# Optimization experiments

Measured on AMD Instinct MI355X. Metric: run time of the kernel, lower is better.

## Reference

```python
import jax, jax.numpy as jnp
import numpy as np

N_HEAD, D_MODEL, D_K, D_V = 8, 128, 16, 16
EPS = 1e-5


def entmax15(x):
    # 1.5-entmax along last axis (Peters & Martins 2019, exact sort-based algo)
    x = x * 0.5
    x = x - jnp.max(x, axis=-1, keepdims=True)
    xs = jnp.flip(jnp.sort(x, axis=-1), axis=-1)  # descending
    K = x.shape[-1]
    rho = jnp.arange(1, K + 1, dtype=x.dtype)
    mean = jnp.cumsum(xs, axis=-1) / rho
    mean_sq = jnp.cumsum(xs * xs, axis=-1) / rho
    delta = (1.0 - rho * (mean_sq - mean * mean)) / rho
    tau = mean - jnp.sqrt(jnp.clip(delta, 0.0))
    support = jnp.sum(tau <= xs, axis=-1, keepdims=True)  # support size k*
    tau_star = jnp.take_along_axis(tau, support - 1, axis=-1)
    p = jnp.clip(x - tau_star, 0.0)
    return p * p


def layer_norm(x, gamma, beta):
    mu = jnp.mean(x, axis=-1, keepdims=True)
    var = jnp.mean((x - mu) ** 2, axis=-1, keepdims=True)
    return gamma * (x - mu) * jax.lax.rsqrt(var + EPS) + beta


def setup_inputs() -> dict:
    key = jax.random.key(0)
    ks = jax.random.split(key, 24)
    B, Lq, Lk, D = 4, 1024, 2048, D_MODEL
    s = 0.05
    f = jax.random.normal
    return {
        "q": f(ks[0], (B, Lq, D), jnp.float32),
        "k": f(ks[1], (B, Lk, D), jnp.float32),
        "v": f(ks[2], (B, Lk, D), jnp.float32),
        "v_2": f(ks[3], (B, Lq, D), jnp.float32),
        "W_Q": f(ks[4], (D, N_HEAD * D_K)) * s, "b_Q": f(ks[5], (N_HEAD * D_K,)) * s,
        "W_K": f(ks[6], (D, N_HEAD * D_K)) * s, "b_K": f(ks[7], (N_HEAD * D_K,)) * s,
        "W_V": f(ks[8], (D, N_HEAD * D_V)) * s, "b_V": f(ks[9], (N_HEAD * D_V,)) * s,
        "W_V2": f(ks[10], (D, N_HEAD * D_V)) * s, "b_V2": f(ks[11], (N_HEAD * D_V,)) * s,
        "W_O": f(ks[12], (N_HEAD * D_V, D)) * s, "b_O": f(ks[13], (D,)) * s,
        "W_O2": f(ks[14], (N_HEAD * D_V, D)) * s, "b_O2": f(ks[15], (D,)) * s,
        "W_R": f(ks[16], (D, D)) * s,
        "W_R2": f(ks[17], (D, D)) * s,
        "gamma": jnp.ones((D,), jnp.float32),
        "beta": jnp.zeros((D,), jnp.float32),
    }


def reference(q, k, v, v_2, W_Q, b_Q, W_K, b_K, W_V, b_V, W_V2, b_V2,
              W_O, b_O, W_O2, b_O2, W_R, W_R2, gamma, beta):
    B, Lq, _ = q.shape
    Lk = k.shape[1]
    Q = (q @ W_Q + b_Q).reshape(B, Lq, N_HEAD, D_K)
    Kh = (k @ W_K + b_K).reshape(B, Lk, N_HEAD, D_K)
    V = (v @ W_V + b_V).reshape(B, Lk, N_HEAD, D_V)
    V2 = (v_2 @ W_V2 + b_V2).reshape(B, Lq, N_HEAD, D_V)
    # scores: [B, H, Lq, Lk]
    scores = jnp.einsum('bqhd,bkhd->bhqk', Q, Kh) / np.float32(np.sqrt(D_K))
    A = entmax15(scores)                              # normalize over Lk
    A2 = entmax15(jnp.swapaxes(scores, -2, -1))       # normalize over Lq
    out = jnp.einsum('bhqk,bkhd->bqhd', A, V).reshape(B, Lq, N_HEAD * D_V)
    out2 = jnp.einsum('bhkq,bqhd->bkhd', A2, V2).reshape(B, Lk, N_HEAD * D_V)
    # dropout is identity in eval mode; both branches use the SAME layer_norm params (as in source)
    out = jax.nn.relu(layer_norm(out @ W_O + b_O + q @ W_R, gamma, beta))
    out2 = jax.nn.relu(layer_norm(out2 @ W_O2 + b_O2 + k @ W_R2, gamma, beta))
    return (out, out2, A, A2)
```

## Files before the change

### kernel.cpp

```cpp
#include <hip/hip_runtime.h>

__global__ __launch_bounds__(128) void proj_all_kernel(
    const float* __restrict__ q, const float* __restrict__ k,
    const float* __restrict__ v, const float* __restrict__ v2,
    const float* __restrict__ W_Q, const float* __restrict__ b_Q,
    const float* __restrict__ W_K, const float* __restrict__ b_K,
    const float* __restrict__ W_V, const float* __restrict__ b_V,
    const float* __restrict__ W_V2, const float* __restrict__ b_V2,
    float* __restrict__ Qp, float* __restrict__ Kp,
    float* __restrict__ Vp, float* __restrict__ V2p)
{
  __shared__ float xs[4][128];
  int blk = blockIdx.x;
  const float *X, *W, *B; float* Y; int L, chunked, rb;
  if (blk < 1024)      { X = q;  W = W_Q;  B = b_Q;  Y = Qp;  L = 1024; chunked = 1; rb = blk; }
  else if (blk < 3072) { X = k;  W = W_K;  B = b_K;  Y = Kp;  L = 2048; chunked = 1; rb = blk - 1024; }
  else if (blk < 5120) { X = v;  W = W_V;  B = b_V;  Y = Vp;  L = 2048; chunked = 0; rb = blk - 3072; }
  else                 { X = v2; W = W_V2; B = b_V2; Y = V2p; L = 1024; chunked = 0; rb = blk - 5120; }
  rb *= 4;
  int c = threadIdx.x;
#pragma unroll
  for (int i = 0; i < 4; ++i)
    xs[i][c] = X[(size_t)(rb + i) * 128 + c];
  __syncthreads();
  float b = B[c];
  float a0 = b, a1 = b, a2 = b, a3 = b;
#pragma unroll 8
  for (int d = 0; d < 128; ++d) {
    float w = W[d * 128 + c];
    a0 = fmaf(xs[0][d], w, a0);
    a1 = fmaf(xs[1][d], w, a1);
    a2 = fmaf(xs[2][d], w, a2);
    a3 = fmaf(xs[3][d], w, a3);
  }
  int h = c >> 4, dd = c & 15;
  float av[4] = { a0, a1, a2, a3 };
#pragma unroll
  for (int i = 0; i < 4; ++i) {
    int row = rb + i;
    int bb = row / L;
    int l  = row - bb * L;
    if (chunked)
      Y[(((size_t)(bb * 8 + h) * 4 + (dd >> 2)) * L + l) * 4 + (dd & 3)] = av[i];
    else
      Y[((size_t)(bb * 8 + h) * L + l) * 16 + dd] = av[i];
  }
}

static __device__ __forceinline__ float hstep(float f, float s1, float cnt)
{
  float arg = fmaf(-cnt, f, s1 * s1);
  return (arg > 0.f) ? f / (s1 + sqrtf(arg)) : f / (2.f * s1);
}

template<int LROW, int LCOL>
__global__ __launch_bounds__(256) void attn_kernel(
    const float* __restrict__ RowM, const float* __restrict__ ColM,
    const float* __restrict__ ValM, float* __restrict__ Aout,
    float* __restrict__ OutWs)
{
  constexpr int J   = LCOL / 64;
  constexpr int CAP = 512;
  constexpr float Z = 1.0f;
  __shared__ float          sval[4][CAP];
  __shared__ unsigned short sidx[4][CAP];

  int ws   = threadIdx.x >> 6;
  int wid  = blockIdx.x * 4 + ws;
  int lane = threadIdx.x & 63;
  int bh   = wid / LROW;
  int r    = wid - bh * LROW;
  int bb   = bh >> 3, h = bh & 7;

  float qf[16];
  { const float* qb = RowM + (size_t)bh * LROW * 16;
#pragma unroll
    for (int d = 0; d < 16; ++d)
      qf[d] = qb[((size_t)(d >> 2) * LROW + r) * 4 + (d & 3)] * 0.125f;
  }

  float x[J];
  const float4* Cb = (const float4*)(ColM + (size_t)bh * LCOL * 16);
#pragma unroll
  for (int j = 0; j < J; ++j) {
    int kk = lane + 64 * j;
    float4 k0 = Cb[0 * LCOL + kk];
    float  s  = qf[0] * k0.x;
    s = fmaf(qf[1], k0.y, s); s = fmaf(qf[2], k0.z, s); s = fmaf(qf[3], k0.w, s);
    float4 k1 = Cb[1 * LCOL + kk];
    s = fmaf(qf[4], k1.x, s); s = fmaf(qf[5], k1.y, s);
    s = fmaf(qf[6], k1.z, s); s = fmaf(qf[7], k1.w, s);
    float4 k2 = Cb[2 * LCOL + kk];
    s = fmaf(qf[8], k2.x, s); s = fmaf(qf[9], k2.y, s);
    s = fmaf(qf[10], k2.z, s); s = fmaf(qf[11], k2.w, s);
    float4 k3 = Cb[3 * LCOL + kk];
    s = fmaf(qf[12], k3.x, s); s = fmaf(qf[13], k3.y, s);
    s = fmaf(qf[14], k3.z, s); s = fmaf(qf[15], k3.w, s);
    x[j] = s;
  }

  float m = -1e30f, sr = 0.f, qr = 0.f;
#pragma unroll
  for (int j = 0; j < J; ++j) {
    m = fmaxf(m, x[j]);
    sr += x[j];
    qr = fmaf(x[j], x[j], qr);
  }
#pragma unroll
  for (int off = 32; off >= 1; off >>= 1) {
    m  = fmaxf(m, __shfl_xor(m, off));
    sr += __shfl_xor(sr, off);
    qr += __shfl_xor(qr, off);
  }
  float mu  = sr * (1.f / (float)LCOL);
  float sig = sqrtf(fmaxf(qr * (1.f / (float)LCOL) - mu * mu, 0.f));
  float theta = fmaxf(fmaf(Z, sig, mu), m - 1.0f);

  float* arow = Aout + ((size_t)bh * LROW + r) * LCOL;
  const float* Vb = ValM + (size_t)bh * LCOL * 16;
  float* op = OutWs + ((size_t)bb * LROW + r) * 128 + h * 16;

  int c = 0;
#pragma unroll
  for (int j = 0; j < J; ++j) c += (x[j] > theta) ? 1 : 0;
  int i = c;
#pragma unroll
  for (int off = 1; off <= 32; off <<= 1) {
    int t = __shfl_up(i, off);
    if (lane >= off) i += t;
  }
  int base = i - c;
  int tot  = __shfl(i, 63);

  if (tot >= 1 && tot <= CAP) {
    int w = 0;
#pragma unroll
    for (int j = 0; j < J; ++j) {
      if (x[j] > theta) {
        sval[ws][base + w] = x[j];
        sidx[ws][base + w] = (unsigned short)(lane + 64 * j);
        ++w;
      }
    }
    __threadfence_block();

    float tau = theta;
    bool valid = true;
    for (int it = 0; it < 24; ++it) {
      float s1 = 0.f, s2 = 0.f;
      int cnt = 0;
      for (int i2 = lane; i2 < tot; i2 += 64) {
        float t = sval[ws][i2] - tau, r0 = fmaxf(t, 0.f);
        s1 += r0; s2 = fmaf(r0, r0, s2);
        cnt += __popcll(__ballot(t > 0.f));
      }
#pragma unroll
      for (int off = 32; off >= 1; off >>= 1) {
        s1 += __shfl_xor(s1, off);
        s2 += __shfl_xor(s2, off);
      }
      float f = s2 - 1.0f;
      if (it == 0 && f < -1e-6f) { valid = false; break; }
      if (f > 1e-6f && s1 > 1e-12f) tau += hstep(f, s1, (float)cnt);
      else break;
    }

    if (valid) {
#pragma unroll
      for (int j = 0; j < J; ++j) {
        int kk = lane + 64 * j;
        float t = fmaxf(x[j] - tau, 0.f);
        arow[kk] = t * t;
      }

      float acc[16];
#pragma unroll
      for (int d = 0; d < 16; ++d) acc[d] = 0.f;
      for (int i2 = lane; i2 < tot; i2 += 64) {
        float t = sval[ws][i2] - tau;
        if (t > 0.f) {
          float p = t * t;
          int kk = sidx[ws][i2];
          const float4* vp = (const float4*)(Vb + (size_t)kk * 16);
          float4 v0 = vp[0], v1 = vp[1], v2 = vp[2], v3 = vp[3];
          acc[0]  = fmaf(p, v0.x, acc[0]);  acc[1]  = fmaf(p, v0.y, acc[1]);
          acc[2]  = fmaf(p, v0.z, acc[2]);  acc[3]  = fmaf(p, v0.w, acc[3]);
          acc[4]  = fmaf(p, v1.x, acc[4]);  acc[5]  = fmaf(p, v1.y, acc[5]);
          acc[6]  = fmaf(p, v1.z, acc[6]);  acc[7]  = fmaf(p, v1.w, acc[7]);
          acc[8]  = fmaf(p, v2.x, acc[8]);  acc[9]  = fmaf(p, v2.y, acc[9]);
          acc[10] = fmaf(p, v2.z, acc[10]); acc[11] = fmaf(p, v2.w, acc[11]);
          acc[12] = fmaf(p, v3.x, acc[12]); acc[13] = fmaf(p, v3.y, acc[13]);
          acc[14] = fmaf(p, v3.z, acc[14]); acc[15] = fmaf(p, v3.w, acc[15]);
        }
      }
#pragma unroll
      for (int off = 32; off >= 1; off >>= 1)
#pragma unroll
        for (int d = 0; d < 16; ++d) acc[d] += __shfl_xor(acc[d], off);
      float vv = acc[0];
#pragma unroll
      for (int d = 1; d < 16; ++d)
        vv = (lane == d) ? acc[d] : vv;
      if (lane < 16) op[lane] = vv;
      return;
    }
  }

  float tau = m - 1.0f;
  bool done = false;
  for (int it = 0; it < 24; ++it) {
    float a1 = 0.f, a2 = 0.f;
    int ac = 0;
#pragma unroll
    for (int j = 0; j < J; ++j) {
      float t = x[j] - tau, r0 = fmaxf(t, 0.f);
      a1 += r0; a2 = fmaf(r0, r0, a2);
      ac += __popcll(__ballot(t > 0.f));
    }
#pragma unroll
    for (int off = 32; off >= 1; off >>= 1) {
      a1 += __shfl_xor(a1, off);
      a2 += __shfl_xor(a2, off);
    }
    float f = a2 - 1.0f;
    bool g = !done && (f > 1e-6f) && (a1 > 1e-12f);
    if (g) tau += hstep(f, a1, (float)ac); else done = true;
    if (done) break;
  }

  float acc[16];
#pragma unroll
  for (int d = 0; d < 16; ++d) acc[d] = 0.f;
#pragma unroll
  for (int j = 0; j < J; ++j) {
    int kk = lane + 64 * j;
    float t = fmaxf(x[j] - tau, 0.f), p = t * t;
    arow[kk] = p;
    const float4* vp = (const float4*)(Vb + (size_t)kk * 16);
    float4 v0 = vp[0], v1 = vp[1], v2 = vp[2], v3 = vp[3];
    acc[0]  = fmaf(p, v0.x, acc[0]);  acc[1]  = fmaf(p, v0.y, acc[1]);
    acc[2]  = fmaf(p, v0.z, acc[2]);  acc[3]  = fmaf(p, v0.w, acc[3]);
    acc[4]  = fmaf(p, v1.x, acc[4]);  acc[5]  = fmaf(p, v1.y, acc[5]);
    acc[6]  = fmaf(p, v1.z, acc[6]);  acc[7]  = fmaf(p, v1.w, acc[7]);
    acc[8]  = fmaf(p, v2.x, acc[8]);  acc[9]  = fmaf(p, v2.y, acc[9]);
    acc[10] = fmaf(p, v2.z, acc[10]); acc[11] = fmaf(p, v2.w, acc[11]);
    acc[12] = fmaf(p, v3.x, acc[12]); acc[13] = fmaf(p, v3.y, acc[13]);
    acc[14] = fmaf(p, v3.z, acc[14]); acc[15] = fmaf(p, v3.w, acc[15]);
  }
#pragma unroll
  for (int off = 32; off >= 1; off >>= 1)
#pragma unroll
    for (int d = 0; d < 16; ++d) acc[d] += __shfl_xor(acc[d], off);
  float vv = acc[0];
#pragma unroll
  for (int d = 1; d < 16; ++d)
    vv = (lane == d) ? acc[d] : vv;
  if (lane < 16) op[lane] = vv;
}

__global__ __launch_bounds__(128) void combine_ln_kernel(
    const float* __restrict__ X1, const float* __restrict__ X2,
    const float* __restrict__ W1, const float* __restrict__ W2,
    const float* __restrict__ bias, const float* __restrict__ gamma,
    const float* __restrict__ beta, float* __restrict__ O)
{
  __shared__ float x1s[4][128], x2s[4][128];
  __shared__ float red[2][8];
  int rb = blockIdx.x * 4;
  int c  = threadIdx.x;
#pragma unroll
  for (int i = 0; i < 4; ++i) {
    x1s[i][c] = X1[(size_t)(rb + i) * 128 + c];
    x2s[i][c] = X2[(size_t)(rb + i) * 128 + c];
  }
  __syncthreads();
  float b = bias[c];
  float a0 = b, a1 = b, a2 = b, a3 = b;
#pragma unroll 8
  for (int d = 0; d < 128; ++d) {
    float w1 = W1[d * 128 + c];
    float w2 = W2[d * 128 + c];
    a0 = fmaf(x1s[0][d], w1, fmaf(x2s[0][d], w2, a0));
    a1 = fmaf(x1s[1][d], w1, fmaf(x2s[1][d], w2, a1));
    a2 = fmaf(x1s[2][d], w1, fmaf(x2s[2][d], w2, a2));
    a3 = fmaf(x1s[3][d], w1, fmaf(x2s[3][d], w2, a3));
  }
  float s0 = a0, s1 = a1, s2 = a2, s3 = a3;
  float q0 = a0 * a0, q1 = a1 * a1, q2 = a2 * a2, q3 = a3 * a3;
#pragma unroll
  for (int off = 32; off >= 1; off >>= 1) {
    s0 += __shfl_xor(s0, off); q0 += __shfl_xor(q0, off);
    s1 += __shfl_xor(s1, off); q1 += __shfl_xor(q1, off);
    s2 += __shfl_xor(s2, off); q2 += __shfl_xor(q2, off);
    s3 += __shfl_xor(s3, off); q3 += __shfl_xor(q3, off);
  }
  int wv = c >> 6;
  if ((c & 63) == 0) {
    red[wv][0] = s0; red[wv][1] = q0; red[wv][2] = s1; red[wv][3] = q1;
    red[wv][4] = s2; red[wv][5] = q2; red[wv][6] = s3; red[wv][7] = q3;
  }
  __syncthreads();
  float S0 = red[0][0] + red[1][0], Q0 = red[0][1] + red[1][1];
  float S1 = red[0][2] + red[1][2], Q1 = red[0][3] + red[1][3];
  float S2 = red[0][4] + red[1][4], Q2 = red[0][5] + red[1][5];
  float S3 = red[0][6] + red[1][6], Q3 = red[0][7] + red[1][7];
  float g = gamma[c], be = beta[c];
  float mu, var, rs;
  mu = S0 * (1.f / 128.f); var = fmaxf(Q0 * (1.f / 128.f) - mu * mu, 0.f);
  rs = rsqrtf(var + 1e-5f);
  O[(size_t)(rb + 0) * 128 + c] = fmaxf(fmaf((a0 - mu) * rs, g, be), 0.f);
  mu = S1 * (1.f / 128.f); var = fmaxf(Q1 * (1.f / 128.f) - mu * mu, 0.f);
  rs = rsqrtf(var + 1e-5f);
  O[(size_t)(rb + 1) * 128 + c] = fmaxf(fmaf((a1 - mu) * rs, g, be), 0.f);
  mu = S2 * (1.f / 128.f); var = fmaxf(Q2 * (1.f / 128.f) - mu * mu, 0.f);
  rs = rsqrtf(var + 1e-5f);
  O[(size_t)(rb + 2) * 128 + c] = fmaxf(fmaf((a2 - mu) * rs, g, be), 0.f);
  mu = S3 * (1.f / 128.f); var = fmaxf(Q3 * (1.f / 128.f) - mu * mu, 0.f);
  rs = rsqrtf(var + 1e-5f);
  O[(size_t)(rb + 3) * 128 + c] = fmaxf(fmaf((a3 - mu) * rs, g, be), 0.f);
}

extern "C"
__attribute__((visibility("default"), used))
void kernel_launch(void* const* d_in, const int* in_sizes, int n_in,
                   void* d_out, int out_size, void* d_ws, size_t ws_size,
                   hipStream_t stream)
{
  (void)in_sizes; (void)n_in; (void)out_size; (void)ws_size;
  const float* q     = (const float*)d_in[0];
  const float* k     = (const float*)d_in[1];
  const float* v     = (const float*)d_in[2];
  const float* v2    = (const float*)d_in[3];
  const float* W_Q   = (const float*)d_in[4];
  const float* b_Q   = (const float*)d_in[5];
  const float* W_K   = (const float*)d_in[6];
  const float* b_K   = (const float*)d_in[7];
  const float* W_V   = (const float*)d_in[8];
  const float* b_V   = (const float*)d_in[9];
  const float* W_V2  = (const float*)d_in[10];
  const float* b_V2  = (const float*)d_in[11];
  const float* W_O   = (const float*)d_in[12];
  const float* b_O   = (const float*)d_in[13];
  const float* W_O2  = (const float*)d_in[14];
  const float* b_O2  = (const float*)d_in[15];
  const float* W_R   = (const float*)d_in[16];
  const float* W_R2  = (const float*)d_in[17];
  const float* gamma = (const float*)d_in[18];
  const float* beta  = (const float*)d_in[19];

  char* ws = (char*)d_ws;
  const size_t MB = 1u << 20;
  float* Qp    = (float*)(ws + 0);
  float* Kp    = (float*)(ws + 2 * MB);
  float* Vp    = (float*)(ws + 6 * MB);
  float* V2p   = (float*)(ws + 10 * MB);
  float* outm1 = (float*)(ws + 12 * MB);
  float* outm2 = (float*)(ws + 14 * MB);

  float* out1  = (float*)d_out;
  float* out2  = out1 + (size_t)524288;
  float* Aout  = out1 + (size_t)1572864;
  float* A2out = out1 + (size_t)68681728;

  proj_all_kernel<<<6144, 128, 0, stream>>>(
      q, k, v, v2, W_Q, b_Q, W_K, b_K, W_V, b_V, W_V2, b_V2,
      Qp, Kp, Vp, V2p);

  attn_kernel<1024, 2048><<<8192,  256, 0, stream>>>(Qp, Kp, Vp,  Aout,  outm1);
  attn_kernel<2048, 1024><<<16384, 256, 0, stream>>>(Kp, Qp, V2p, A2out, outm2);

  combine_ln_kernel<<<1024, 128, 0, stream>>>(outm1, q, W_O,  W_R,  b_O,
                                              gamma, beta, out1);
  combine_ln_kernel<<<2048, 128, 0, stream>>>(outm2, k, W_O2, W_R2, b_O2,
                                              gamma, beta, out2);
}
```

Baseline: 1.066 ms.

## Stage key tiles in LDS shared by eight row-waves per block

The attention kernel now runs eight waves per block, each handling one row of the same batch-head, and cooperatively loads 512-key tiles into shared memory. All waves reuse those tiles for the score dot products, which cuts redundant global and L2 reads of the column matrix. The sparse-support scratch arrays alias the same shared buffer after a barrier. This adds block-wide syncs and larger blocks, which can lower occupancy and serialise the load and compute phases.

```diff
diff --git a/kernel.cpp b/kernel.cpp
--- a/kernel.cpp
+++ b/kernel.cpp
@@ -54,22 +54,30 @@
 }
 
 template<int LROW, int LCOL>
-__global__ __launch_bounds__(256) void attn_kernel(
+__global__ __launch_bounds__(512) void attn_kernel(
     const float* __restrict__ RowM, const float* __restrict__ ColM,
     const float* __restrict__ ValM, float* __restrict__ Aout,
     float* __restrict__ OutWs)
 {
   constexpr int J   = LCOL / 64;
+  constexpr int T   = 512;
+  constexpr int NT  = LCOL / T;
+  constexpr int JT  = T / 64;
   constexpr int CAP = 512;
   constexpr float Z = 1.0f;
-  __shared__ float          sval[4][CAP];
-  __shared__ unsigned short sidx[4][CAP];
-
-  int ws   = threadIdx.x >> 6;
-  int wid  = blockIdx.x * 4 + ws;
-  int lane = threadIdx.x & 63;
-  int bh   = wid / LROW;
-  int r    = wid - bh * LROW;
+
+  __shared__ __align__(16) char smem[32 * 1024];
+  float4*         ldsK  = (float4*)smem;
+  float*          svalb = (float*)smem;
+  unsigned short* sidxb = (unsigned short*)(smem + 16 * 1024);
+
+  int tid  = threadIdx.x;
+  int ws   = tid >> 6;
+  int lane = tid & 63;
+  int nrg  = LROW / 8;
+  int bh   = blockIdx.x / nrg;
+  int rg   = blockIdx.x - bh * nrg;
+  int r    = rg * 8 + ws;
   int bb   = bh >> 3, h = bh & 7;
 
   float qf[16];
@@ -81,23 +89,31 @@
 
   float x[J];
   const float4* Cb = (const float4*)(ColM + (size_t)bh * LCOL * 16);
-#pragma unroll
-  for (int j = 0; j < J; ++j) {
-    int kk = lane + 64 * j;
-    float4 k0 = Cb[0 * LCOL + kk];
-    float  s  = qf[0] * k0.x;
-    s = fmaf(qf[1], k0.y, s); s = fmaf(qf[2], k0.z, s); s = fmaf(qf[3], k0.w, s);
-    float4 k1 = Cb[1 * LCOL + kk];
-    s = fmaf(qf[4], k1.x, s); s = fmaf(qf[5], k1.y, s);
-    s = fmaf(qf[6], k1.z, s); s = fmaf(qf[7], k1.w, s);
-    float4 k2 = Cb[2 * LCOL + kk];
-    s = fmaf(qf[8], k2.x, s); s = fmaf(qf[9], k2.y, s);
-    s = fmaf(qf[10], k2.z, s); s = fmaf(qf[11], k2.w, s);
-    float4 k3 = Cb[3 * LCOL + kk];
-    s = fmaf(qf[12], k3.x, s); s = fmaf(qf[13], k3.y, s);
-    s = fmaf(qf[14], k3.z, s); s = fmaf(qf[15], k3.w, s);
-    x[j] = s;
-  }
+  for (int t = 0; t < NT; ++t) {
+    __syncthreads();
+#pragma unroll
+    for (int e = 0; e < 4; ++e)
+      ldsK[e * T + tid] = Cb[(size_t)e * LCOL + t * T + tid];
+    __syncthreads();
+#pragma unroll
+    for (int jt = 0; jt < JT; ++jt) {
+      int kl = lane + 64 * jt;
+      float4 k0 = ldsK[0 * T + kl];
+      float4 k1 = ldsK[1 * T + kl];
+      float4 k2 = ldsK[2 * T + kl];
+      float4 k3 = ldsK[3 * T + kl];
+      float s = qf[0] * k0.x;
+      s = fmaf(qf[1],  k0.y, s); s = fmaf(qf[2],  k0.z, s); s = fmaf(qf[3],  k0.w, s);
+      s = fmaf(qf[4],  k1.x, s); s = fmaf(qf[5],  k1.y, s);
+      s = fmaf(qf[6],  k1.z, s); s = fmaf(qf[7],  k1.w, s);
+      s = fmaf(qf[8],  k2.x, s); s = fmaf(qf[9],  k2.y, s);
+      s = fmaf(qf[10], k2.z, s); s = fmaf(qf[11], k2.w, s);
+      s = fmaf(qf[12], k3.x, s); s = fmaf(qf[13], k3.y, s);
+      s = fmaf(qf[14], k3.z, s); s = fmaf(qf[15], k3.w, s);
+      x[t * JT + jt] = s;
+    }
+  }
+  __syncthreads();
 
   float m = -1e30f, sr = 0.f, qr = 0.f;
 #pragma unroll
@@ -132,13 +148,16 @@
   int base = i - c;
   int tot  = __shfl(i, 63);
 
+  float* sval = svalb + ws * CAP;
+  unsigned short* sidx = sidxb + ws * CAP;
+
   if (tot >= 1 && tot <= CAP) {
     int w = 0;
 #pragma unroll
     for (int j = 0; j < J; ++j) {
       if (x[j] > theta) {
-        sval[ws][base + w] = x[j];
-        sidx[ws][base + w] = (unsigned short)(lane + 64 * j);
+        sval[base + w] = x[j];
+        sidx[base + w] = (unsigned short)(lane + 64 * j);
         ++w;
       }
     }
@@ -150,7 +169,7 @@
       float s1 = 0.f, s2 = 0.f;
       int cnt = 0;
       for (int i2 = lane; i2 < tot; i2 += 64) {
-        float t = sval[ws][i2] - tau, r0 = fmaxf(t, 0.f);
+        float t = sval[i2] - tau, r0 = fmaxf(t, 0.f);
         s1 += r0; s2 = fmaf(r0, r0, s2);
         cnt += __popcll(__ballot(t > 0.f));
       }
@@ -177,10 +196,10 @@
 #pragma unroll
       for (int d = 0; d < 16; ++d) acc[d] = 0.f;
       for (int i2 = lane; i2 < tot; i2 += 64) {
-        float t = sval[ws][i2] - tau;
+        float t = sval[i2] - tau;
         if (t > 0.f) {
           float p = t * t;
-          int kk = sidx[ws][i2];
+          int kk = sidx[i2];
           const float4* vp = (const float4*)(Vb + (size_t)kk * 16);
           float4 v0 = vp[0], v1 = vp[1], v2 = vp[2], v3 = vp[3];
           acc[0]  = fmaf(p, v0.x, acc[0]);  acc[1]  = fmaf(p, v0.y, acc[1]);
@@ -366,8 +385,8 @@
       q, k, v, v2, W_Q, b_Q, W_K, b_K, W_V, b_V, W_V2, b_V2,
       Qp, Kp, Vp, V2p);
 
-  attn_kernel<1024, 2048><<<8192,  256, 0, stream>>>(Qp, Kp, Vp,  Aout,  outm1);
-  attn_kernel<2048, 1024><<<16384, 256, 0, stream>>>(Kp, Qp, V2p, A2out, outm2);
+  attn_kernel<1024, 2048><<<4096, 512, 0, stream>>>(Qp, Kp, Vp,  Aout,  outm1);
+  attn_kernel<2048, 1024><<<8192, 512, 0, stream>>>(Kp, Qp, V2p, A2out, outm2);
 
   combine_ln_kernel<<<1024, 128, 0, stream>>>(outm1, q, W_O,  W_R,  b_O,
                                               gamma, beta, out1);
```

Result: slower. 1.096 ms (+2.8%).
